# Kernel tuning notes

Hardware: AMD Instinct MI355X
Metric: run time of the kernel (lower is better)

The kernel has to match this reference:

```python
import jax, jax.numpy as jnp
import numpy as np

MIN_BW = 0.1
MAX_BW = 10.0
BW_FACTOR = 1.0
SAMPLE = 512  # min(512, B) with B >= 512


def _pairwise_dist_sq(a, b):
    # ||a_i - b_j||^2 via GEMM: [N, M], avoids [N, M, D] intermediate
    a2 = jnp.sum(a * a, axis=-1)[:, None]
    b2 = jnp.sum(b * b, axis=-1)[None, :]
    d = a2 + b2 - 2.0 * (a @ b.T)
    return jnp.maximum(d, 0.0)


def _bandwidth(x, y):
    # torch: median heuristic on first SAMPLE rows, under no_grad
    xs = jax.lax.stop_gradient(x[:SAMPLE])
    ys = jax.lax.stop_gradient(y[:SAMPLE])
    dist_sq = _pairwise_dist_sq(xs, ys)
    bw_sq = jnp.median(dist_sq.reshape(-1))
    bw = jnp.sqrt(bw_sq / 2.0) * BW_FACTOR
    return jnp.clip(bw, MIN_BW, MAX_BW)


def setup_inputs() -> dict:
    key = jax.random.key(0)
    kx, ksx, ky, ksy = jax.random.split(key, 4)
    B, D = 4096, 512
    return {
        "x": jax.random.normal(kx, (B, D), dtype=jnp.float32),
        "score_x": jax.random.normal(ksx, (B, D), dtype=jnp.float32),
        "y": jax.random.normal(ky, (B, D), dtype=jnp.float32),
        "score_y": jax.random.normal(ksy, (B, D), dtype=jnp.float32),
    }


def reference(x, score_x, y, score_y):
    D = x.shape[-1]
    h = _bandwidth(x, y)
    h2 = h * h

    dist_sq = _pairwise_dist_sq(x, y)                      # [B, B]
    k = jnp.exp(-dist_sq / (2.0 * h2))                     # [B, B]

    # term1[i,j] = k[i,j] * <score_x_i, score_y_j>
    term1 = k * (score_x @ score_y.T)

    # term2[i,j] = <x_i - y_j, score_y_j> * k[i,j] / h^2
    term2 = ((x @ score_y.T) - jnp.sum(y * score_y, axis=-1)[None, :]) * k / h2

    # term3[i,j] = ||x_i - y_j||^2 * k / h^4 - k * D / h^2
    term3 = dist_sq * k / (h2 * h2) - k * (D / h2)

    return term1 + term2 + term3
```

## Files before the change

### kernel.cpp

```cpp
#include <hip/hip_runtime.h>
#include <hip/hip_bf16.h>

typedef __attribute__((ext_vector_type(8))) short bf16x8;
typedef __attribute__((ext_vector_type(4))) float f32x4;

#define B_N 4096
#define DIM 512
#define HBINS 8192

#define OFF_PARAMS 0
#define OFF_X2     256
#define OFF_Y2     16640
#define OFF_YSY    33024
#define OFF_HIST   49408
#define OFF_TILES  98304
#define MAT_ELEMS  2097152
#define WS_NEED    (OFF_TILES + (size_t)4 * MAT_ELEMS * 2)

static __device__ __forceinline__ unsigned short f2bf_rne(float f) {
    unsigned int u = __float_as_uint(f);
    u += 0x7FFFu + ((u >> 16) & 1u);
    return (unsigned short)(u >> 16);
}
static __device__ __forceinline__ float bf2f(unsigned short h) {
    return __uint_as_float(((unsigned int)h) << 16);
}

static __device__ __forceinline__ int swz(int r, int k) {
    return r * 32 + ((((k >> 3) ^ ((r >> 1) & 3))) << 3) + (k & 7);
}

static __device__ __forceinline__ void median_from_lds(
    unsigned int* hsum, unsigned int* part, float* vv, int t) {
    unsigned int s = 0;
#pragma unroll 8
    for (int b = t * 32; b < t * 32 + 32; ++b) s += hsum[b];
    part[t] = s;
    __syncthreads();
    unsigned int pre = 0;
    for (int i = 0; i < 256; ++i) {
        unsigned int v = part[i];
        if (i < t) pre += v;
    }
    const unsigned int kk1 = 131072u, kk2 = 131073u;
    unsigned int hi = pre + s;
#pragma unroll
    for (int sel = 0; sel < 2; ++sel) {
        unsigned int kk = sel ? kk2 : kk1;
        if (kk > pre && kk <= hi) {
            unsigned int cc = pre;
            for (int b = 0; b < 32; ++b) {
                cc += hsum[t * 32 + b];
                if (cc >= kk) { vv[sel] = ((float)(t * 32 + b) + 0.5f) * 0.25f; break; }
            }
        }
    }
    __syncthreads();
}


__global__ __launch_bounds__(256) void k_preAll(
    const float* __restrict__ X, const float* __restrict__ Y,
    const float* __restrict__ SY, unsigned short* __restrict__ tiles,
    float* __restrict__ x2, float* __restrict__ y2, float* __restrict__ ysy,
    unsigned int* __restrict__ hist) {
    __shared__ __align__(16) unsigned short sAB[4096];
    __shared__ unsigned int hloc[HBINS];
    __shared__ float rn[128];

    int b = blockIdx.x, t = threadIdx.x;

    if (b < 512) {
        int side = b >> 8;
        int tile = (b & 255) >> 3;
        int ky = b & 7;
        unsigned short* base0 = tiles + (size_t)side * 2 * MAT_ELEMS;
        unsigned short* base1 = base0 + MAT_ELEMS;
#pragma unroll
        for (int kt2 = 0; kt2 < 2; ++kt2) {
            int kt = ky * 2 + kt2;
            unsigned short* d0 = base0 + (size_t)(tile * 16 + kt) * 4096;
            unsigned short* d1 = base1 + (size_t)(tile * 16 + kt) * 4096;
#pragma unroll
            for (int c = 0; c < 2; ++c) {
                int v = c * 256 + t;
                int r = (v >> 6) * 16 + (v & 15);
                int k = ((v >> 4) & 3) << 3;
                const float* gp = (side ? Y : X) + (size_t)(tile * 128 + r) * DIM + kt * 32 + k;
                float4 p0 = *(const float4*)gp;
                float4 p1 = *(const float4*)(gp + 4);
                float pv[8] = {p0.x, p0.y, p0.z, p0.w, p1.x, p1.y, p1.z, p1.w};
                float s1 = 0.f, s2 = 0.f;
                bf16x8 h0;
                if (side) {
                    const float* gq = SY + (size_t)(tile * 128 + r) * DIM + kt * 32 + k;
                    float4 q0 = *(const float4*)gq;
                    float4 q1 = *(const float4*)(gq + 4);
                    float qv[8] = {q0.x, q0.y, q0.z, q0.w, q1.x, q1.y, q1.z, q1.w};
                    bf16x8 h1;
#pragma unroll
                    for (int j = 0; j < 8; ++j) {
                        s1 += pv[j] * pv[j];
                        s2 += pv[j] * qv[j];
                        h0[j] = (short)f2bf_rne(pv[j]);
                        h1[j] = (short)f2bf_rne(qv[j]);
                    }
                    *(bf16x8*)&d1[v * 8] = h1;
                } else {
#pragma unroll
                    for (int j = 0; j < 8; ++j) {
                        s1 += pv[j] * pv[j];
                        h0[j] = (short)f2bf_rne(pv[j]);
                    }
                }
                *(bf16x8*)&d0[v * 8] = h0;
                s1 += __shfl_xor(s1, 16); s1 += __shfl_xor(s1, 32);
                if (side) { s2 += __shfl_xor(s2, 16); s2 += __shfl_xor(s2, 32); }
                if ((t & 48) == 0) {
                    int row = tile * 128 + r;
                    if (side == 0) {
                        atomicAdd(&x2[row], s1);
                    } else {
                        atomicAdd(&y2[row], s1);
                        atomicAdd(&ysy[row], s2);
                    }
                }
            }
        }
    } else {
        unsigned short* sA = &sAB[0];
        unsigned short* sB = &sAB[2048];
        float* x2s = &rn[0];
        float* y2s = &rn[64];
        int hb = b - 512;
        int bi = hb >> 3, bj = hb & 7;
        for (int i = t; i < HBINS; i += 256) hloc[i] = 0;

        int lane = t & 63, w = t >> 6;
        int wm = w >> 1, wn = w & 1;
        int fr = lane & 15, fko = (lane >> 4) * 8;

        f32x4 axy[2][2];
#pragma unroll
        for (int i = 0; i < 2; ++i)
#pragma unroll
            for (int j = 0; j < 2; ++j) axy[i][j] = (f32x4)0.f;

        int r = t >> 2, k0 = (t & 3) * 8;
        const float* gx = X + (size_t)(bi * 64 + r) * DIM + k0;
        const float* gy = Y + (size_t)(bj * 64 + r) * DIM + k0;

        int ixA[2], ixB[2];
#pragma unroll
        for (int fm = 0; fm < 2; ++fm) ixA[fm] = swz(wm * 32 + fm * 16 + fr, fko);
#pragma unroll
        for (int fn = 0; fn < 2; ++fn) ixB[fn] = swz(wn * 32 + fn * 16 + fr, fko);

        float na = 0.f, nb = 0.f;
        float4 A0, A1, B0, B1;
#define LDK(kt_) do {                                                       \
            A0 = *(const float4*)(gx + (kt_) * 32);                         \
            A1 = *(const float4*)(gx + (kt_) * 32 + 4);                     \
            B0 = *(const float4*)(gy + (kt_) * 32);                         \
            B1 = *(const float4*)(gy + (kt_) * 32 + 4);                     \
        } while (0)

        LDK(0);
        for (int kt = 0; kt < 16; ++kt) {
            float av[8] = {A0.x, A0.y, A0.z, A0.w, A1.x, A1.y, A1.z, A1.w};
            float bv[8] = {B0.x, B0.y, B0.z, B0.w, B1.x, B1.y, B1.z, B1.w};
            bf16x8 ha, hb2;
#pragma unroll
            for (int j = 0; j < 8; ++j) {
                na += av[j] * av[j];
                nb += bv[j] * bv[j];
                ha[j] = (short)f2bf_rne(av[j]);
                hb2[j] = (short)f2bf_rne(bv[j]);
            }
            __syncthreads();
            *(bf16x8*)&sA[swz(r, k0)] = ha;
            *(bf16x8*)&sB[swz(r, k0)] = hb2;
            if (kt < 15) LDK(kt + 1);
            __syncthreads();

            bf16x8 aX[2];
#pragma unroll
            for (int fm = 0; fm < 2; ++fm) aX[fm] = *(const bf16x8*)&sA[ixA[fm]];
#pragma unroll
            for (int fn = 0; fn < 2; ++fn) {
                bf16x8 bY = *(const bf16x8*)&sB[ixB[fn]];
#pragma unroll
                for (int fm = 0; fm < 2; ++fm)
                    axy[fm][fn] = __builtin_amdgcn_mfma_f32_16x16x32_bf16(aX[fm], bY, axy[fm][fn], 0, 0, 0);
            }
        }
#undef LDK

        na += __shfl_xor(na, 1); na += __shfl_xor(na, 2);
        nb += __shfl_xor(nb, 1); nb += __shfl_xor(nb, 2);
        if ((t & 3) == 0) { x2s[r] = na; y2s[r] = nb; }
        __syncthreads();

        int fq = lane >> 4;
#pragma unroll
        for (int fm = 0; fm < 2; ++fm)
#pragma unroll
            for (int fn = 0; fn < 2; ++fn)
#pragma unroll
                for (int rr = 0; rr < 4; ++rr) {
                    int rl = wm * 32 + fm * 16 + fq * 4 + rr;
                    int cl = wn * 32 + fn * 16 + fr;
                    float d = fmaxf(x2s[rl] + y2s[cl] - 2.0f * axy[fm][fn][rr], 0.0f);
                    int bin = (int)(d * 4.0f);
                    if (bin > HBINS - 1) bin = HBINS - 1;
                    atomicAdd(&hloc[bin], 1u);
                }
        __syncthreads();
        for (int i = t; i < HBINS; i += 256) {
            unsigned int v = hloc[i];
            if (v) atomicAdd(&hist[i], v);
        }
    }
}

__global__ __launch_bounds__(256) void k_preC(
    const float* __restrict__ X, const float* __restrict__ SX,
    const unsigned int* __restrict__ hist, float* __restrict__ params,
    unsigned short* __restrict__ tiles) {
    __shared__ unsigned int hsum[HBINS];
    __shared__ unsigned int part[256];
    __shared__ float vv[2];
    int t = threadIdx.x;
    for (int i = t; i < HBINS / 4; i += 256)
        ((uint4*)hsum)[i] = ((const uint4*)hist)[i];
    __syncthreads();
    median_from_lds(hsum, part, vv, t);
    float med = 0.5f * (vv[0] + vv[1]);
    float bw = fminf(fmaxf(sqrtf(med * 0.5f), 0.1f), 10.0f);
    float h2 = bw * bw;
    float c1 = 1.0f / h2;
    if (blockIdx.x == 0 && blockIdx.y == 0 && t == 0) {
        params[0] = 1.0f / (2.0f * h2);
        params[1] = c1;
        params[2] = 1.0f / (h2 * h2);
        params[3] = (float)DIM / h2;
    }

    int tile = blockIdx.x;
    unsigned short* base1 = tiles + MAT_ELEMS;
#pragma unroll
    for (int kt2 = 0; kt2 < 2; ++kt2) {
        int kt = blockIdx.y * 2 + kt2;
        unsigned short* d1 = base1 + (size_t)(tile * 16 + kt) * 4096;
#pragma unroll
        for (int c = 0; c < 2; ++c) {
            int v = c * 256 + t;
            int r = (v >> 6) * 16 + (v & 15);
            int k = ((v >> 4) & 3) << 3;
            const float* gp = X + (size_t)(tile * 128 + r) * DIM + kt * 32 + k;
            const float* gq = SX + (size_t)(tile * 128 + r) * DIM + kt * 32 + k;
            float4 p0 = *(const float4*)gp;
            float4 p1 = *(const float4*)(gp + 4);
            float4 q0 = *(const float4*)gq;
            float4 q1 = *(const float4*)(gq + 4);
            float pv[8] = {p0.x, p0.y, p0.z, p0.w, p1.x, p1.y, p1.z, p1.w};
            float qv[8] = {q0.x, q0.y, q0.z, q0.w, q1.x, q1.y, q1.z, q1.w};
            bf16x8 h1;
#pragma unroll
            for (int j = 0; j < 8; ++j) h1[j] = (short)f2bf_rne(qv[j] + c1 * pv[j]);
            *(bf16x8*)&d1[v * 8] = h1;
        }
    }
}

#define GLD(g, l) __builtin_amdgcn_global_load_lds(                                   \
    (const __attribute__((address_space(1))) void*)(g),                               \
    (__attribute__((address_space(3))) void*)(l), 16, 0, 0)

__global__ __launch_bounds__(256, 2) void k_main(
    const unsigned short* __restrict__ tiles,
    const float* __restrict__ x2g, const float* __restrict__ y2g,
    const float* __restrict__ ysyg, const float* __restrict__ params,
    float* __restrict__ out) {
    __shared__ __align__(16) unsigned short sA[3][4096];
    __shared__ __align__(16) unsigned short sB[3][4096];
    __shared__ float x2s[128], y2s[128], ysys[128];

    int t = threadIdx.x;
    int bm = blockIdx.y, bn = blockIdx.x;
    if (t < 128) x2s[t] = x2g[bm * 128 + t];
    else { y2s[t - 128] = y2g[bn * 128 + (t - 128)]; ysys[t - 128] = ysyg[bn * 128 + (t - 128)]; }
    __syncthreads();

    int lane = t & 63, w = t >> 6;
    int wm = w >> 1, wn = w & 1;

    f32x4 axy[4][4], acb[4][4];
#pragma unroll
    for (int i = 0; i < 4; ++i)
#pragma unroll
        for (int j = 0; j < 4; ++j) { axy[i][j] = (f32x4)0.f; acb[i][j] = (f32x4)0.f; }

    const unsigned short* gaX = tiles + (size_t)(bm * 16) * 4096 + t * 8;
    const unsigned short* gbY = tiles + (size_t)2 * MAT_ELEMS + (size_t)(bn * 16) * 4096 + t * 8;
    const unsigned short* gaC = tiles + (size_t)MAT_ELEMS + (size_t)(bm * 16) * 4096
                              + (wm * 4) * 512 + lane * 8;
    const unsigned short* gbS = tiles + (size_t)3 * MAT_ELEMS + (size_t)(bn * 16) * 4096
                              + (wn * 4) * 512 + lane * 8;

#define STAGE(buf, kt_) do {                                                     \
        const unsigned short* pa_ = gaX + (size_t)(kt_) * 4096;                  \
        const unsigned short* pb_ = gbY + (size_t)(kt_) * 4096;                  \
        GLD(pa_,        &sA[buf][t * 8]);                                        \
        GLD(pa_ + 2048, &sA[buf][2048 + t * 8]);                                 \
        GLD(pb_,        &sB[buf][t * 8]);                                        \
        GLD(pb_ + 2048, &sB[buf][2048 + t * 8]);                                 \
    } while (0)

#define FRAGLD(dC, dS, kt_) do {                                                 \
        const unsigned short* pc_ = gaC + (size_t)(kt_) * 4096;                  \
        const unsigned short* ps_ = gbS + (size_t)(kt_) * 4096;                  \
        dC[0] = *(const bf16x8*)(pc_);        dS[0] = *(const bf16x8*)(ps_);     \
        dC[1] = *(const bf16x8*)(pc_ + 512);  dS[1] = *(const bf16x8*)(ps_ + 512);\
        dC[2] = *(const bf16x8*)(pc_ + 1024); dS[2] = *(const bf16x8*)(ps_ + 1024);\
        dC[3] = *(const bf16x8*)(pc_ + 1536); dS[3] = *(const bf16x8*)(ps_ + 1536);\
    } while (0)

    int ixA[4], ixB[4];
#pragma unroll
    for (int fm = 0; fm < 4; ++fm) ixA[fm] = (wm * 4 + fm) * 512 + lane * 8;
#pragma unroll
    for (int fn = 0; fn < 4; ++fn) ixB[fn] = (wn * 4 + fn) * 512 + lane * 8;

    bf16x8 fC0[4], fS0[4], fC1[4], fS1[4];

#define KSTEP(CB, CURC, CURS, NXTC, NXTS, SKT, FKT, MODE, WAITN) do {            \
        asm volatile("s_waitcnt vmcnt(" #WAITN ")" ::: "memory");                \
        __builtin_amdgcn_sched_barrier(0);                                       \
        __builtin_amdgcn_s_barrier();                                            \
        __builtin_amdgcn_sched_barrier(0);                                       \
        if (MODE >= 1) FRAGLD(NXTC, NXTS, FKT);                                  \
        if (MODE == 2) STAGE(((CB) + 2) % 3, SKT);                               \
        bf16x8 dX[4], dY[4];                                                     \
        dX[0] = *(const bf16x8*)&sA[CB][ixA[0]];                                 \
        dX[1] = *(const bf16x8*)&sA[CB][ixA[1]];                                 \
        dX[2] = *(const bf16x8*)&sA[CB][ixA[2]];                                 \
        dX[3] = *(const bf16x8*)&sA[CB][ixA[3]];                                 \
        dY[0] = *(const bf16x8*)&sB[CB][ixB[0]];                                 \
        dY[1] = *(const bf16x8*)&sB[CB][ixB[1]];                                 \
        dY[2] = *(const bf16x8*)&sB[CB][ixB[2]];                                 \
        dY[3] = *(const bf16x8*)&sB[CB][ixB[3]];                                 \
        __builtin_amdgcn_s_setprio(1);                                           \
        _Pragma("unroll")                                                        \
        for (int fn_ = 0; fn_ < 4; ++fn_) {                                      \
            _Pragma("unroll")                                                    \
            for (int fm_ = 0; fm_ < 4; ++fm_) {                                  \
                axy[fm_][fn_] = __builtin_amdgcn_mfma_f32_16x16x32_bf16(         \
                    dX[fm_], dY[fn_], axy[fm_][fn_], 0, 0, 0);                   \
                acb[fm_][fn_] = __builtin_amdgcn_mfma_f32_16x16x32_bf16(         \
                    CURC[fm_], CURS[fn_], acb[fm_][fn_], 0, 0, 0);               \
            }                                                                    \
        }                                                                        \
        __builtin_amdgcn_s_setprio(0);                                           \
        __builtin_amdgcn_sched_barrier(0);                                       \
    } while (0)

    STAGE(0, 0);
    FRAGLD(fC0, fS0, 0);
    STAGE(1, 1);

    for (int k6 = 0; k6 < 2; ++k6) {
        int kt = k6 * 6;
        KSTEP(0, fC0, fS0, fC1, fS1, kt + 2, kt + 1, 2, 12);
        KSTEP(1, fC1, fS1, fC0, fS0, kt + 3, kt + 2, 2, 12);
        KSTEP(2, fC0, fS0, fC1, fS1, kt + 4, kt + 3, 2, 12);
        KSTEP(0, fC1, fS1, fC0, fS0, kt + 5, kt + 4, 2, 12);
        KSTEP(1, fC0, fS0, fC1, fS1, kt + 6, kt + 5, 2, 12);
        KSTEP(2, fC1, fS1, fC0, fS0, kt + 7, kt + 6, 2, 12);
    }
    KSTEP(0, fC0, fS0, fC1, fS1, 14, 13, 2, 12);
    KSTEP(1, fC1, fS1, fC0, fS0, 15, 14, 2, 12);
    KSTEP(2, fC0, fS0, fC1, fS1, 0, 15, 1, 12);
    KSTEP(0, fC1, fS1, fC0, fS0, 0, 0, 0, 8);
#undef KSTEP
#undef STAGE
#undef FRAGLD

    float c0 = params[0], c1 = params[1], c2 = params[2], c3 = params[3];
    int fr = lane & 15, fq = lane >> 4;
#pragma unroll
    for (int fm = 0; fm < 4; ++fm) {
#pragma unroll
        for (int fn = 0; fn < 4; ++fn) {
#pragma unroll
            for (int r = 0; r < 4; ++r) {
                int rl = wm * 64 + fm * 16 + fq * 4 + r;
                int cl = wn * 64 + fn * 16 + fr;
                float d = fmaxf(x2s[rl] + y2s[cl] - 2.0f * axy[fm][fn][r], 0.0f);
                float kv = __expf(-d * c0);
                out[(size_t)(bm * 128 + rl) * B_N + (bn * 128 + cl)] =
                    kv * (acb[fm][fn][r] - c1 * ysys[cl] + d * c2 - c3);
            }
        }
    }
}

__global__ void k_rowstats(const float* __restrict__ X, const float* __restrict__ Y,
                           const float* __restrict__ SY,
                           float* __restrict__ x2, float* __restrict__ y2,
                           float* __restrict__ ysy) {
    int t = threadIdx.x;
    int r = blockIdx.x * 4 + (t >> 6);
    int lane = t & 63;
    const float4* px = (const float4*)(X + (size_t)r * DIM) + lane * 2;
    const float4* py = (const float4*)(Y + (size_t)r * DIM) + lane * 2;
    const float4* ps = (const float4*)(SY + (size_t)r * DIM) + lane * 2;
    float4 a0 = px[0], a1 = px[1];
    float4 b0 = py[0], b1 = py[1];
    float4 c0 = ps[0], c1 = ps[1];
    float s1 = a0.x*a0.x + a0.y*a0.y + a0.z*a0.z + a0.w*a0.w
             + a1.x*a1.x + a1.y*a1.y + a1.z*a1.z + a1.w*a1.w;
    float s2 = b0.x*b0.x + b0.y*b0.y + b0.z*b0.z + b0.w*b0.w
             + b1.x*b1.x + b1.y*b1.y + b1.z*b1.z + b1.w*b1.w;
    float s3 = b0.x*c0.x + b0.y*c0.y + b0.z*c0.z + b0.w*c0.w
             + b1.x*c1.x + b1.y*c1.y + b1.z*c1.z + b1.w*c1.w;
#pragma unroll
    for (int o = 32; o > 0; o >>= 1) {
        s1 += __shfl_down(s1, o);
        s2 += __shfl_down(s2, o);
        s3 += __shfl_down(s3, o);
    }
    if (lane == 0) { x2[r] = s1; y2[r] = s2; ysy[r] = s3; }
}

__global__ void k_hist_fp32(const float* __restrict__ X, const float* __restrict__ Y,
                            const float* __restrict__ x2, const float* __restrict__ y2,
                            unsigned int* __restrict__ hist) {
    __shared__ float xs[32][68];
    __shared__ float ys[32][68];
    __shared__ unsigned int hloc[HBINS];
    int t = threadIdx.x;
    for (int i = t; i < HBINS; i += 256) hloc[i] = 0;
    int i0 = blockIdx.y * 32, j0 = blockIdx.x * 32;
    float a00 = 0.f, a01 = 0.f, a10 = 0.f, a11 = 0.f;
    int ti = (t >> 4) * 2, tj = (t & 15) * 2;
    for (int c = 0; c < 8; ++c) {
        __syncthreads();
        int rr = t >> 3, cc = (t & 7) * 8;
        const float* gx = X + (size_t)(i0 + rr) * DIM + c * 64 + cc;
        *(float4*)&xs[rr][cc] = *(const float4*)gx;
        *(float4*)&xs[rr][cc + 4] = *(const float4*)(gx + 4);
        const float* gy = Y + (size_t)(j0 + rr) * DIM + c * 64 + cc;
        *(float4*)&ys[rr][cc] = *(const float4*)gy;
        *(float4*)&ys[rr][cc + 4] = *(const float4*)(gy + 4);
        __syncthreads();
        for (int kk = 0; kk < 64; ++kk) {
            float a0 = xs[ti][kk], a1 = xs[ti + 1][kk];
            float b0 = ys[tj][kk], b1 = ys[tj + 1][kk];
            a00 += a0 * b0; a01 += a0 * b1; a10 += a1 * b0; a11 += a1 * b1;
        }
    }
    float s[2][2] = {{a00, a01}, {a10, a11}};
#pragma unroll
    for (int ii = 0; ii < 2; ++ii)
#pragma unroll
        for (int jj = 0; jj < 2; ++jj) {
            float d = fmaxf(x2[i0 + ti + ii] + y2[j0 + tj + jj] - 2.f * s[ii][jj], 0.f);
            int bin = (int)(d * 4.0f);
            if (bin > HBINS - 1) bin = HBINS - 1;
            atomicAdd(&hloc[bin], 1u);
        }
    __syncthreads();
    for (int i = t; i < HBINS; i += 256) {
        unsigned int v = hloc[i];
        if (v) atomicAdd(&hist[i], v);
    }
}

__global__ __launch_bounds__(256, 1) void k_median(
    const unsigned int* __restrict__ hist, float* __restrict__ params) {
    __shared__ unsigned int hsum[HBINS];
    __shared__ unsigned int part[256];
    __shared__ float vv[2];
    int t = threadIdx.x;
    for (int i = t; i < HBINS / 4; i += 256)
        ((uint4*)hsum)[i] = ((const uint4*)hist)[i];
    __syncthreads();
    median_from_lds(hsum, part, vv, t);
    if (t == 0) {
        float med = 0.5f * (vv[0] + vv[1]);
        float bw = fminf(fmaxf(sqrtf(med * 0.5f), 0.1f), 10.0f);
        float h2 = bw * bw;
        params[0] = 1.0f / (2.0f * h2);
        params[1] = 1.0f / h2;
        params[2] = 1.0f / (h2 * h2);
        params[3] = (float)DIM / h2;
    }
}

static __device__ __forceinline__ void store_hi(unsigned short* tile, int r, int k0,
                                                float4 v0, float4 v1) {
    bf16x8 h;
    h[0] = (short)f2bf_rne(v0.x); h[1] = (short)f2bf_rne(v0.y);
    h[2] = (short)f2bf_rne(v0.z); h[3] = (short)f2bf_rne(v0.w);
    h[4] = (short)f2bf_rne(v1.x); h[5] = (short)f2bf_rne(v1.y);
    h[6] = (short)f2bf_rne(v1.z); h[7] = (short)f2bf_rne(v1.w);
    *(bf16x8*)&tile[swz(r, k0)] = h;
}
static __device__ __forceinline__ void store_hilo(unsigned short* th, unsigned short* tl,
                                                  int r, int k0, float4 v0, float4 v1) {
    float f[8] = {v0.x, v0.y, v0.z, v0.w, v1.x, v1.y, v1.z, v1.w};
    bf16x8 h, l;
#pragma unroll
    for (int j = 0; j < 8; ++j) {
        unsigned short hh = f2bf_rne(f[j]);
        h[j] = (short)hh;
        l[j] = (short)f2bf_rne(f[j] - bf2f(hh));
    }
    *(bf16x8*)&th[swz(r, k0)] = h;
    *(bf16x8*)&tl[swz(r, k0)] = l;
}

__global__ __launch_bounds__(256, 2) void k_main_fb(
    const float* __restrict__ X, const float* __restrict__ SX,
    const float* __restrict__ Y, const float* __restrict__ SY,
    const float* __restrict__ x2g, const float* __restrict__ y2g,
    const float* __restrict__ ysyg, const float* __restrict__ params,
    float* __restrict__ out) {
    __shared__ __align__(16) unsigned short tX[4096];
    __shared__ __align__(16) unsigned short tSXH[4096];
    __shared__ __align__(16) unsigned short tSXL[4096];
    __shared__ __align__(16) unsigned short tY[2048];
    __shared__ __align__(16) unsigned short tSYH[2048];
    __shared__ __align__(16) unsigned short tSYL[2048];
    __shared__ float x2s[128];
    __shared__ float y2s[64];
    __shared__ float ysys[64];

    int t = threadIdx.x;
    int bm = blockIdx.y, bn = blockIdx.x;
    if (t < 128) x2s[t] = x2g[bm * 128 + t];
    else if (t < 192) y2s[t - 128] = y2g[bn * 64 + (t - 128)];
    else ysys[t - 192] = ysyg[bn * 64 + (t - 192)];

    int lane = t & 63, w = t >> 6, wm = w >> 1, wn = w & 1;
    f32x4 axy[4][2], ass[4][2], axsy[4][2];
#pragma unroll
    for (int i = 0; i < 4; ++i)
#pragma unroll
        for (int j = 0; j < 2; ++j) {
            axy[i][j] = (f32x4)0.f; ass[i][j] = (f32x4)0.f; axsy[i][j] = (f32x4)0.f;
        }

    for (int kt = 0; kt < DIM / 32; ++kt) {
        int kb = kt * 32;
#pragma unroll
        for (int h = 0; h < 2; ++h) {
            int s = t + h * 256;
            int r = s >> 2, k0 = (s & 3) * 8;
            const float* gx = X + (size_t)(bm * 128 + r) * DIM + kb + k0;
            store_hi(tX, r, k0, *(const float4*)gx, *(const float4*)(gx + 4));
            const float* gs = SX + (size_t)(bm * 128 + r) * DIM + kb + k0;
            store_hilo(tSXH, tSXL, r, k0, *(const float4*)gs, *(const float4*)(gs + 4));
        }
        {
            int r = t >> 2, k0 = (t & 3) * 8;
            const float* gy = Y + (size_t)(bn * 64 + r) * DIM + kb + k0;
            store_hi(tY, r, k0, *(const float4*)gy, *(const float4*)(gy + 4));
            const float* gq = SY + (size_t)(bn * 64 + r) * DIM + kb + k0;
            store_hilo(tSYH, tSYL, r, k0, *(const float4*)gq, *(const float4*)(gq + 4));
        }
        __syncthreads();

        int fr = lane & 15, fk = (lane >> 4) * 8;
        bf16x8 aX[4], aSH[4], aSL[4];
#pragma unroll
        for (int fm = 0; fm < 4; ++fm) {
            int ix = swz(wm * 64 + fm * 16 + fr, fk);
            aX[fm] = *(const bf16x8*)&tX[ix];
            aSH[fm] = *(const bf16x8*)&tSXH[ix];
            aSL[fm] = *(const bf16x8*)&tSXL[ix];
        }
#pragma unroll
        for (int fn = 0; fn < 2; ++fn) {
            int iy = swz(wn * 32 + fn * 16 + fr, fk);
            bf16x8 bY = *(const bf16x8*)&tY[iy];
            bf16x8 bH = *(const bf16x8*)&tSYH[iy];
            bf16x8 bL = *(const bf16x8*)&tSYL[iy];
#pragma unroll
            for (int fm = 0; fm < 4; ++fm) {
                axy[fm][fn] = __builtin_amdgcn_mfma_f32_16x16x32_bf16(aX[fm], bY, axy[fm][fn], 0, 0, 0);
                ass[fm][fn] = __builtin_amdgcn_mfma_f32_16x16x32_bf16(aSH[fm], bH, ass[fm][fn], 0, 0, 0);
                ass[fm][fn] = __builtin_amdgcn_mfma_f32_16x16x32_bf16(aSH[fm], bL, ass[fm][fn], 0, 0, 0);
                ass[fm][fn] = __builtin_amdgcn_mfma_f32_16x16x32_bf16(aSL[fm], bH, ass[fm][fn], 0, 0, 0);
                axsy[fm][fn] = __builtin_amdgcn_mfma_f32_16x16x32_bf16(aX[fm], bH, axsy[fm][fn], 0, 0, 0);
            }
        }
        __syncthreads();
    }

    float c0 = params[0], c1 = params[1], c2 = params[2], c3 = params[3];
    int fr = lane & 15, fq = lane >> 4;
#pragma unroll
    for (int fm = 0; fm < 4; ++fm)
#pragma unroll
        for (int fn = 0; fn < 2; ++fn)
#pragma unroll
            for (int r = 0; r < 4; ++r) {
                int rl = wm * 64 + fm * 16 + fq * 4 + r;
                int cl = wn * 32 + fn * 16 + fr;
                float d = fmaxf(x2s[rl] + y2s[cl] - 2.0f * axy[fm][fn][r], 0.0f);
                float kv = __expf(-d * c0);
                out[(size_t)(bm * 128 + rl) * B_N + (bn * 64 + cl)] =
                    kv * ass[fm][fn][r] + (axsy[fm][fn][r] - ysys[cl]) * (kv * c1)
                    + d * kv * c2 - kv * c3;
            }
}

extern "C" void kernel_launch(void* const* d_in, const int* in_sizes, int n_in,
                              void* d_out, int out_size, void* d_ws, size_t ws_size,
                              hipStream_t stream) {
    const float* x  = (const float*)d_in[0];
    const float* sx = (const float*)d_in[1];
    const float* y  = (const float*)d_in[2];
    const float* sy = (const float*)d_in[3];
    float* out = (float*)d_out;
    char* ws = (char*)d_ws;
    float* params = (float*)(ws + OFF_PARAMS);
    float* x2 = (float*)(ws + OFF_X2);
    float* y2 = (float*)(ws + OFF_Y2);
    float* ysy = (float*)(ws + OFF_YSY);
    unsigned int* hist = (unsigned int*)(ws + OFF_HIST);
    unsigned short* tiles = (unsigned short*)(ws + OFF_TILES);

    if (ws_size >= WS_NEED) {
        hipMemsetAsync(ws + OFF_X2, 0, 3 * 16384 + HBINS * 4, stream);
        k_preAll<<<576, 256, 0, stream>>>(x, y, sy, tiles, x2, y2, ysy, hist);
        k_preC<<<dim3(32, 8), 256, 0, stream>>>(x, sx, hist, params, tiles);
        k_main<<<dim3(32, 32), dim3(256), 0, stream>>>(tiles, x2, y2, ysy, params, out);
    } else {
        hipMemsetAsync(hist, 0, HBINS * 4, stream);
        k_rowstats<<<B_N / 4, 256, 0, stream>>>(x, y, sy, x2, y2, ysy);
        k_hist_fp32<<<dim3(16, 16), dim3(256), 0, stream>>>(x, y, x2, y2, hist);
        k_median<<<1, 256, 0, stream>>>(hist, params);
        k_main_fb<<<dim3(64, 32), dim3(256), 0, stream>>>(x, sx, y, sy, x2, y2, ysy, params, out);
    }
}
```

Baseline: 83.64 us.

## Halve k_main N-tile to 64 and switch to double-buffered pipeline

The main fused GEMM kernel now computes 128x64 output tiles instead of 128x128, launching twice as many blocks (2048 vs 1024) with half the accumulators per wave. The LDS ring shrinks from triple to double buffering with a simpler uniform prefetch loop, and launch bounds are raised to target 3 blocks per CU. The aim is better occupancy and load balance across CUs. The cost is less data reuse, since the X and score_x tiles are now loaded twice as often, and a shallower prefetch depth.

```diff
diff --git a/kernel.cpp b/kernel.cpp
--- a/kernel.cpp
+++ b/kernel.cpp
@@ -277,36 +277,39 @@
     (const __attribute__((address_space(1))) void*)(g),                               \
     (__attribute__((address_space(3))) void*)(l), 16, 0, 0)
 
-__global__ __launch_bounds__(256, 2) void k_main(
+__global__ __launch_bounds__(256, 3) void k_main(
     const unsigned short* __restrict__ tiles,
     const float* __restrict__ x2g, const float* __restrict__ y2g,
     const float* __restrict__ ysyg, const float* __restrict__ params,
     float* __restrict__ out) {
-    __shared__ __align__(16) unsigned short sA[3][4096];
-    __shared__ __align__(16) unsigned short sB[3][4096];
-    __shared__ float x2s[128], y2s[128], ysys[128];
+    __shared__ __align__(16) unsigned short sA[2][4096];
+    __shared__ __align__(16) unsigned short sB[2][2048];
+    __shared__ float x2s[128], y2s[64], ysys[64];
 
     int t = threadIdx.x;
     int bm = blockIdx.y, bn = blockIdx.x;
     if (t < 128) x2s[t] = x2g[bm * 128 + t];
-    else { y2s[t - 128] = y2g[bn * 128 + (t - 128)]; ysys[t - 128] = ysyg[bn * 128 + (t - 128)]; }
+    else if (t < 192) y2s[t - 128] = y2g[bn * 64 + (t - 128)];
+    else ysys[t - 192] = ysyg[bn * 64 + (t - 192)];
     __syncthreads();
 
     int lane = t & 63, w = t >> 6;
     int wm = w >> 1, wn = w & 1;
 
-    f32x4 axy[4][4], acb[4][4];
+    f32x4 axy[4][2], acb[4][2];
 #pragma unroll
     for (int i = 0; i < 4; ++i)
 #pragma unroll
-        for (int j = 0; j < 4; ++j) { axy[i][j] = (f32x4)0.f; acb[i][j] = (f32x4)0.f; }
-
+        for (int j = 0; j < 2; ++j) { axy[i][j] = (f32x4)0.f; acb[i][j] = (f32x4)0.f; }
+
+    int tileB = bn >> 1, half = bn & 1;
     const unsigned short* gaX = tiles + (size_t)(bm * 16) * 4096 + t * 8;
-    const unsigned short* gbY = tiles + (size_t)2 * MAT_ELEMS + (size_t)(bn * 16) * 4096 + t * 8;
+    const unsigned short* gbY = tiles + (size_t)2 * MAT_ELEMS + (size_t)(tileB * 16) * 4096
+                              + half * 2048 + t * 8;
     const unsigned short* gaC = tiles + (size_t)MAT_ELEMS + (size_t)(bm * 16) * 4096
                               + (wm * 4) * 512 + lane * 8;
-    const unsigned short* gbS = tiles + (size_t)3 * MAT_ELEMS + (size_t)(bn * 16) * 4096
-                              + (wn * 4) * 512 + lane * 8;
+    const unsigned short* gbS = tiles + (size_t)3 * MAT_ELEMS + (size_t)(tileB * 16) * 4096
+                              + half * 2048 + (wn * 2) * 512 + lane * 8;
 
 #define STAGE(buf, kt_) do {                                                     \
         const unsigned short* pa_ = gaX + (size_t)(kt_) * 4096;                  \
@@ -314,45 +317,46 @@
         GLD(pa_,        &sA[buf][t * 8]);                                        \
         GLD(pa_ + 2048, &sA[buf][2048 + t * 8]);                                 \
         GLD(pb_,        &sB[buf][t * 8]);                                        \
-        GLD(pb_ + 2048, &sB[buf][2048 + t * 8]);                                 \
     } while (0)
 
 #define FRAGLD(dC, dS, kt_) do {                                                 \
         const unsigned short* pc_ = gaC + (size_t)(kt_) * 4096;                  \
         const unsigned short* ps_ = gbS + (size_t)(kt_) * 4096;                  \
-        dC[0] = *(const bf16x8*)(pc_);        dS[0] = *(const bf16x8*)(ps_);     \
-        dC[1] = *(const bf16x8*)(pc_ + 512);  dS[1] = *(const bf16x8*)(ps_ + 512);\
-        dC[2] = *(const bf16x8*)(pc_ + 1024); dS[2] = *(const bf16x8*)(ps_ + 1024);\
-        dC[3] = *(const bf16x8*)(pc_ + 1536); dS[3] = *(const bf16x8*)(ps_ + 1536);\
+        dC[0] = *(const bf16x8*)(pc_);                                           \
+        dC[1] = *(const bf16x8*)(pc_ + 512);                                     \
+        dC[2] = *(const bf16x8*)(pc_ + 1024);                                    \
+        dC[3] = *(const bf16x8*)(pc_ + 1536);                                    \
+        dS[0] = *(const bf16x8*)(ps_);                                           \
+        dS[1] = *(const bf16x8*)(ps_ + 512);                                     \
     } while (0)
 
-    int ixA[4], ixB[4];
+    int ixA[4], ixB[2];
 #pragma unroll
     for (int fm = 0; fm < 4; ++fm) ixA[fm] = (wm * 4 + fm) * 512 + lane * 8;
 #pragma unroll
-    for (int fn = 0; fn < 4; ++fn) ixB[fn] = (wn * 4 + fn) * 512 + lane * 8;
-
-    bf16x8 fC0[4], fS0[4], fC1[4], fS1[4];
-
-#define KSTEP(CB, CURC, CURS, NXTC, NXTS, SKT, FKT, MODE, WAITN) do {            \
-        asm volatile("s_waitcnt vmcnt(" #WAITN ")" ::: "memory");                \
+    for (int fn = 0; fn < 2; ++fn) ixB[fn] = (wn * 2 + fn) * 512 + lane * 8;
+
+    bf16x8 fC0[4], fS0[2], fC1[4], fS1[2];
+
+#define KSTEP(CB, CURC, CURS, NXTC, NXTS, NKT, DOPF) do {                        \
+        asm volatile("s_waitcnt vmcnt(6)" ::: "memory");   \
         __builtin_amdgcn_sched_barrier(0);                                       \
         __builtin_amdgcn_s_barrier();                                            \
         __builtin_amdgcn_sched_barrier(0);                                       \
-        if (MODE >= 1) FRAGLD(NXTC, NXTS, FKT);                                  \
-        if (MODE == 2) STAGE(((CB) + 2) % 3, SKT);                               \
-        bf16x8 dX[4], dY[4];                                                     \
+        if (DOPF) {                                                              \
+            STAGE(CB ^ 1, NKT);                                                  \
+            FRAGLD(NXTC, NXTS, NKT);                                             \
+        }                                                                        \
+        bf16x8 dX[4], dY[2];                                                     \
         dX[0] = *(const bf16x8*)&sA[CB][ixA[0]];                                 \
         dX[1] = *(const bf16x8*)&sA[CB][ixA[1]];                                 \
         dX[2] = *(const bf16x8*)&sA[CB][ixA[2]];                                 \
         dX[3] = *(const bf16x8*)&sA[CB][ixA[3]];                                 \
         dY[0] = *(const bf16x8*)&sB[CB][ixB[0]];                                 \
         dY[1] = *(const bf16x8*)&sB[CB][ixB[1]];                                 \
-        dY[2] = *(const bf16x8*)&sB[CB][ixB[2]];                                 \
-        dY[3] = *(const bf16x8*)&sB[CB][ixB[3]];                                 \
         __builtin_amdgcn_s_setprio(1);                                           \
         _Pragma("unroll")                                                        \
-        for (int fn_ = 0; fn_ < 4; ++fn_) {                                      \
+        for (int fn_ = 0; fn_ < 2; ++fn_) {                                      \
             _Pragma("unroll")                                                    \
             for (int fm_ = 0; fm_ < 4; ++fm_) {                                  \
                 axy[fm_][fn_] = __builtin_amdgcn_mfma_f32_16x16x32_bf16(         \
@@ -367,21 +371,13 @@
 
     STAGE(0, 0);
     FRAGLD(fC0, fS0, 0);
-    STAGE(1, 1);
-
-    for (int k6 = 0; k6 < 2; ++k6) {
-        int kt = k6 * 6;
-        KSTEP(0, fC0, fS0, fC1, fS1, kt + 2, kt + 1, 2, 12);
-        KSTEP(1, fC1, fS1, fC0, fS0, kt + 3, kt + 2, 2, 12);
-        KSTEP(2, fC0, fS0, fC1, fS1, kt + 4, kt + 3, 2, 12);
-        KSTEP(0, fC1, fS1, fC0, fS0, kt + 5, kt + 4, 2, 12);
-        KSTEP(1, fC0, fS0, fC1, fS1, kt + 6, kt + 5, 2, 12);
-        KSTEP(2, fC1, fS1, fC0, fS0, kt + 7, kt + 6, 2, 12);
-    }
-    KSTEP(0, fC0, fS0, fC1, fS1, 14, 13, 2, 12);
-    KSTEP(1, fC1, fS1, fC0, fS0, 15, 14, 2, 12);
-    KSTEP(2, fC0, fS0, fC1, fS1, 0, 15, 1, 12);
-    KSTEP(0, fC1, fS1, fC0, fS0, 0, 0, 0, 8);
+
+    for (int k2 = 0; k2 < 7; ++k2) {
+        KSTEP(0, fC0, fS0, fC1, fS1, 2 * k2 + 1, 1);
+        KSTEP(1, fC1, fS1, fC0, fS0, 2 * k2 + 2, 1);
+    }
+    KSTEP(0, fC0, fS0, fC1, fS1, 15, 1);
+    KSTEP(1, fC1, fS1, fC0, fS0, 0, 0);
 #undef KSTEP
 #undef STAGE
 #undef FRAGLD
@@ -391,14 +387,14 @@
 #pragma unroll
     for (int fm = 0; fm < 4; ++fm) {
 #pragma unroll
-        for (int fn = 0; fn < 4; ++fn) {
+        for (int fn = 0; fn < 2; ++fn) {
 #pragma unroll
             for (int r = 0; r < 4; ++r) {
                 int rl = wm * 64 + fm * 16 + fq * 4 + r;
-                int cl = wn * 64 + fn * 16 + fr;
+                int cl = wn * 32 + fn * 16 + fr;
                 float d = fmaxf(x2s[rl] + y2s[cl] - 2.0f * axy[fm][fn][r], 0.0f);
                 float kv = __expf(-d * c0);
-                out[(size_t)(bm * 128 + rl) * B_N + (bn * 128 + cl)] =
+                out[(size_t)(bm * 128 + rl) * B_N + (bn * 64 + cl)] =
                     kv * (acb[fm][fn][r] - c1 * ysys[cl] + d * c2 - c3);
             }
         }
@@ -637,7 +633,7 @@
         hipMemsetAsync(ws + OFF_X2, 0, 3 * 16384 + HBINS * 4, stream);
         k_preAll<<<576, 256, 0, stream>>>(x, y, sy, tiles, x2, y2, ysy, hist);
         k_preC<<<dim3(32, 8), 256, 0, stream>>>(x, sx, hist, params, tiles);
-        k_main<<<dim3(32, 32), dim3(256), 0, stream>>>(tiles, x2, y2, ysy, params, out);
+        k_main<<<dim3(64, 32), dim3(256), 0, stream>>>(tiles, x2, y2, ysy, params, out);
     } else {
         hipMemsetAsync(hist, 0, HBINS * 4, stream);
         k_rowstats<<<B_N / 4, 256, 0, stream>>>(x, y, sy, x2, y2, ysy);
```

New measurement: 86.86 us. 1.04x slower.
